# Optimization experiments

Hardware: AMD Instinct MI355X
Metric: run time of the kernel (lower is better)

The kernel has to match this reference:

```python
import jax, jax.numpy as jnp
import numpy as np

N = 6144   # number of patches (bag size)
L = 1024   # input feature dim
D = 512    # GCN hidden dim
ALPHA = 0.4
THRESH = 0.5


def _layernorm(x, g, b):
    m = jnp.mean(x, axis=-1, keepdims=True)
    v = jnp.mean((x - m) ** 2, axis=-1, keepdims=True)
    return (x - m) / jnp.sqrt(v + 1e-5) * g + b


def _l1rows(x):
    # F.normalize(x, p=1): row-wise L1 normalize with eps=1e-12
    return x / jnp.maximum(jnp.sum(jnp.abs(x), axis=1, keepdims=True), 1e-12)


def _nonlin(x, w1, b1, g, bn, w2, b2):
    h = jax.nn.relu(_layernorm(x @ w1 + b1, g, bn))
    return h @ w2 + b2


def _gcn(x, adj, w, b, g, bn):
    # GraphConvolution: adj @ (x @ W) + bias, then LayerNorm + ReLU
    return jax.nn.relu(_layernorm(adj @ (x @ w) + b, g, bn))


def setup_inputs() -> dict:
    key = jax.random.key(0)
    ks = iter(jax.random.split(key, 64))

    def nrm(shape, s=0.02):
        return jax.random.normal(next(ks), shape, jnp.float32) * s

    inp = {
        'x_path': jax.random.normal(next(ks), (N, L), jnp.float32),
        'maps': jax.random.uniform(next(ks), (N, N), jnp.float32) * 0.1,
    }
    for pre in ['nl0', 'nl1']:
        inp[pre + '_w1'] = nrm((L, D)); inp[pre + '_b1'] = jnp.zeros((D,), jnp.float32)
        inp[pre + '_g'] = jnp.ones((D,), jnp.float32); inp[pre + '_bn'] = jnp.zeros((D,), jnp.float32)
        inp[pre + '_w2'] = nrm((D, D)); inp[pre + '_b2'] = jnp.zeros((D,), jnp.float32)
    for pre in ['gc0', 'gc1', 'gc2', 'ga0', 'ga1', 'ga2']:
        inp[pre + '_w'] = nrm((D, D)); inp[pre + '_b'] = jnp.zeros((D,), jnp.float32)
        inp[pre + '_g'] = jnp.ones((D,), jnp.float32); inp[pre + '_bn'] = jnp.zeros((D,), jnp.float32)
    inp['attn_wa'] = nrm((L, 256)); inp['attn_ba'] = jnp.zeros((256,), jnp.float32)
    inp['attn_wb'] = nrm((L, 256)); inp['attn_bb'] = jnp.zeros((256,), jnp.float32)
    inp['attn_wc'] = nrm((256, 1)); inp['attn_bc'] = jnp.zeros((1,), jnp.float32)
    inp['cls_w'] = nrm((L, 4), 0.001)
    inp['ln_g'] = jnp.ones((L,), jnp.float32); inp['ln_b'] = jnp.zeros((L,), jnp.float32)
    return inp


def reference(x_path, maps,
              nl0_w1, nl0_b1, nl0_g, nl0_bn, nl0_w2, nl0_b2,
              nl1_w1, nl1_b1, nl1_g, nl1_bn, nl1_w2, nl1_b2,
              gc0_w, gc0_b, gc0_g, gc0_bn,
              gc1_w, gc1_b, gc1_g, gc1_bn,
              gc2_w, gc2_b, gc2_g, gc2_bn,
              ga0_w, ga0_b, ga0_g, ga0_bn,
              ga1_w, ga1_b, ga1_g, ga1_bn,
              ga2_w, ga2_b, ga2_g, ga2_bn,
              attn_wa, attn_ba, attn_wb, attn_bb, attn_wc, attn_bc,
              cls_w, ln_g, ln_b):
    # cosine-similarity adjacency: L2-normalize rows, gram matrix, min-max, threshold
    xn = x_path / jnp.maximum(jnp.linalg.norm(x_path, axis=1, keepdims=True), 1e-12)
    cs = xn @ xn.T                                       # [N,N]
    cs = (cs - cs.min()) / (cs.max() - cs.min())
    cs = (cs >= THRESH).astype(jnp.float32)

    # gated attention (eval mode, no dropout): A = Wc (tanh(Wa x) * sigmoid(Wb x))
    a = jnp.tanh(x_path @ attn_wa + attn_ba)
    bg = jax.nn.sigmoid(x_path @ attn_wb + attn_bb)
    agg = (a * bg) @ attn_wc + attn_bc                   # [N,1]

    s = jax.nn.sigmoid(agg)
    aw = s * s.T                                         # outer product [N,N]
    aw = (aw - aw.min()) / (aw.max() - aw.min())
    aw = ALPHA + (1.0 - ALPHA) * aw + maps

    cs = _l1rows(cs)
    aw = _l1rows(aw)

    x0 = _nonlin(x_path, nl0_w1, nl0_b1, nl0_g, nl0_bn, nl0_w2, nl0_b2)
    x1 = _nonlin(x_path, nl1_w1, nl1_b1, nl1_g, nl1_bn, nl1_w2, nl1_b2)

    g1 = _gcn(x0, cs, gc0_w, gc0_b, gc0_g, gc0_bn)
    g1 = _gcn(g1, cs, gc1_w, gc1_b, gc1_g, gc1_bn)
    g1 = _gcn(g1, cs, gc2_w, gc2_b, gc2_g, gc2_bn)

    g2 = _gcn(x1, aw, ga0_w, ga0_b, ga0_g, ga0_bn)
    g2 = _gcn(g2, aw, ga1_w, ga1_b, ga1_g, ga1_bn)
    g2 = _gcn(g2, aw, ga2_w, ga2_b, ga2_g, ga2_bn)

    gcf = jnp.concatenate([g2, g1], axis=1)              # [N, 1024]

    n = x_path.shape[0]
    trans = (cs @ agg) / (n ** 0.5)                      # [N,1]
    fw = jax.nn.softmax(0.3 * trans + 0.7 * agg, axis=0) # softmax over patches
    pooled = fw.T @ gcf                                  # [1, 1024]
    pooled = _layernorm(pooled, ln_g, ln_b)

    logits = pooled @ cls_w                              # [1, 4]
    y_hat = jnp.argmax(logits, axis=1, keepdims=True)    # topk k=1 index
    hazards = jax.nn.sigmoid(logits)
    surv = jnp.cumprod(1.0 - hazards, axis=1)
    return hazards, surv, y_hat
```

## Files before the change

kernel.cpp:

```cpp
#include <hip/hip_runtime.h>

#define N_ 6144
#define L_ 1024
#define D_ 512
#define H_ 256
#define SPARSE_MAX 64u

typedef unsigned short u16;
typedef unsigned long long u64;
typedef __attribute__((ext_vector_type(4))) float f32x4;
typedef __attribute__((ext_vector_type(8))) short s16x8;
typedef __attribute__((ext_vector_type(4))) short s16x4;

__device__ __forceinline__ u16 f2b(float f){
  unsigned u = __float_as_uint(f);
  u += 0x7FFFu + ((u >> 16) & 1u);
  return (u16)(u >> 16);
}
__device__ __forceinline__ float b2f(u16 h){ return __uint_as_float(((unsigned)h) << 16); }
__device__ __forceinline__ unsigned fkey(float f){
  unsigned u = __float_as_uint(f);
  return (u & 0x80000000u) ? ~u : (u | 0x80000000u);
}
__device__ __forceinline__ float funkey(unsigned k){
  unsigned u = (k & 0x80000000u) ? (k & 0x7FFFFFFFu) : ~k;
  return __uint_as_float(u);
}
__device__ __forceinline__ float wave_sum(float v){
  #pragma unroll
  for(int o=32;o;o>>=1) v += __shfl_xor(v,o);
  return v;
}
__device__ __forceinline__ float wave_max(float v){
  #pragma unroll
  for(int o=32;o;o>>=1) v = fmaxf(v,__shfl_xor(v,o));
  return v;
}
__device__ __forceinline__ float wave_min(float v){
  #pragma unroll
  for(int o=32;o;o>>=1) v = fminf(v,__shfl_xor(v,o));
  return v;
}
__device__ __forceinline__ float blk_sum256(float v){
  __shared__ float sm[4];
  v = wave_sum(v);
  __syncthreads();
  if((threadIdx.x&63)==0) sm[threadIdx.x>>6]=v;
  __syncthreads();
  return sm[0]+sm[1]+sm[2]+sm[3];
}
__device__ __forceinline__ float blk_min256(float v){
  __shared__ float sm[4];
  v = wave_min(v);
  __syncthreads();
  if((threadIdx.x&63)==0) sm[threadIdx.x>>6]=v;
  __syncthreads();
  return fminf(fminf(sm[0],sm[1]),fminf(sm[2],sm[3]));
}
__device__ __forceinline__ float blk_max256(float v){
  __shared__ float sm[4];
  v = wave_max(v);
  __syncthreads();
  if((threadIdx.x&63)==0) sm[threadIdx.x>>6]=v;
  __syncthreads();
  return fmaxf(fmaxf(sm[0],sm[1]),fmaxf(sm[2],sm[3]));
}


template<int VW> __device__ __forceinline__ void waitv(){
  if constexpr(VW==8) asm volatile("s_waitcnt vmcnt(8)" ::: "memory");
  else if constexpr(VW==4) asm volatile("s_waitcnt vmcnt(4)" ::: "memory");
  else asm volatile("s_waitcnt vmcnt(0)" ::: "memory");
}

#define STG4(bb,k0) do{ \
  __builtin_amdgcn_global_load_lds((__attribute__((address_space(1))) void*)(gA0+(k0)), (__attribute__((address_space(3))) void*)(lds + (bb)*4096 + (wid<<9)),        16, 0, 0); \
  __builtin_amdgcn_global_load_lds((__attribute__((address_space(1))) void*)(gA1+(k0)), (__attribute__((address_space(3))) void*)(lds + (bb)*4096 + 2048 + (wid<<9)), 16, 0, 0); \
  __builtin_amdgcn_global_load_lds((__attribute__((address_space(1))) void*)(gB0+(k0)), (__attribute__((address_space(3))) void*)(lds + 12288 + (bb)*4096 + (wid<<9)),        16, 0, 0); \
  __builtin_amdgcn_global_load_lds((__attribute__((address_space(1))) void*)(gB1+(k0)), (__attribute__((address_space(3))) void*)(lds + 12288 + (bb)*4096 + 2048 + (wid<<9)), 16, 0, 0); \
}while(0)

template<int MODE>
__global__ __launch_bounds__(256) void gemm_bt(
  const u16* __restrict__ A, const u16* __restrict__ Bt,
  int M, int Nc, int K,
  u16* __restrict__ Cb, unsigned* __restrict__ mmx,
  const unsigned* __restrict__ gate)
{
  if (gate && gate[2] <= SPARSE_MAX) return;
  __shared__ __align__(16) u16 lds[3*4096*2];
  const int tid = threadIdx.x;
  const int wid = tid>>6, lane = tid&63;

  const int gx = gridDim.x;
  int lid = blockIdx.y*gx + blockIdx.x;
  const int nwg = gx*gridDim.y;
  if ((nwg & 7) == 0) {
    const int chunk = nwg >> 3;
    lid = (lid & 7)*chunk + (lid >> 3);
  }
  const int m0 = (lid/gx)<<7, n0 = (lid%gx)<<7;
  const int wr = wid>>1, wc = wid&1;

  const int Klen = K / gridDim.z;
  const int kbeg = blockIdx.z * Klen;

  const int srow = (wid<<4) + (lane>>2);
  const int scol = (((lane&3) ^ ((lane>>2)&3))<<3);
  const u16* gA0 = A  + (size_t)(m0+srow   )*K + scol;
  const u16* gA1 = A  + (size_t)(m0+srow+64)*K + scol;
  const u16* gB0 = Bt + (size_t)(n0+srow   )*K + scol;
  const u16* gB1 = Bt + (size_t)(n0+srow+64)*K + scol;

  f32x4 acc[4][4] = {};
  const int lr = lane&15, lk = (lane>>4)<<3;
  const int rdo = lk ^ ((lr&3)<<3);

  const int NIT = Klen>>5;
  STG4(0, kbeg);
  STG4(1, kbeg+32);
  STG4(2, kbeg+64);

  for (int it=0; it<NIT-2; ++it){
    const int b = it - (it/3)*3;
    waitv<8>();
    __builtin_amdgcn_s_barrier();
    const u16* baseA = lds + b*4096;
    const u16* baseB = lds + 12288 + b*4096;
    s16x8 af[4], bfr[4];
    #pragma unroll
    for(int m=0;m<4;m++) af[m]  = *(const s16x8*)(baseA + ((wr<<6)+(m<<4)+lr)*32 + rdo);
    #pragma unroll
    for(int n=0;n<4;n++) bfr[n] = *(const s16x8*)(baseB + ((wc<<6)+(n<<4)+lr)*32 + rdo);
    asm volatile("s_waitcnt lgkmcnt(0)" ::: "memory");
    __builtin_amdgcn_sched_barrier(0);
    __builtin_amdgcn_s_barrier();
    if (it+3 < NIT) STG4(b, kbeg + ((it+3)<<5));
    #pragma unroll
    for(int m=0;m<4;m++)
      #pragma unroll
      for(int n=0;n<4;n++)
        acc[m][n] = __builtin_amdgcn_mfma_f32_16x16x32_bf16(af[m], bfr[n], acc[m][n], 0,0,0);
  }
  {
    const int it = NIT-2; const int b = it - (it/3)*3;
    waitv<4>();
    __builtin_amdgcn_s_barrier();
    const u16* baseA = lds + b*4096;
    const u16* baseB = lds + 12288 + b*4096;
    s16x8 af[4], bfr[4];
    #pragma unroll
    for(int m=0;m<4;m++) af[m]  = *(const s16x8*)(baseA + ((wr<<6)+(m<<4)+lr)*32 + rdo);
    #pragma unroll
    for(int n=0;n<4;n++) bfr[n] = *(const s16x8*)(baseB + ((wc<<6)+(n<<4)+lr)*32 + rdo);
    #pragma unroll
    for(int m=0;m<4;m++)
      #pragma unroll
      for(int n=0;n<4;n++)
        acc[m][n] = __builtin_amdgcn_mfma_f32_16x16x32_bf16(af[m], bfr[n], acc[m][n], 0,0,0);
  }
  {
    const int it = NIT-1; const int b = it - (it/3)*3;
    waitv<0>();
    __builtin_amdgcn_s_barrier();
    const u16* baseA = lds + b*4096;
    const u16* baseB = lds + 12288 + b*4096;
    s16x8 af[4], bfr[4];
    #pragma unroll
    for(int m=0;m<4;m++) af[m]  = *(const s16x8*)(baseA + ((wr<<6)+(m<<4)+lr)*32 + rdo);
    #pragma unroll
    for(int n=0;n<4;n++) bfr[n] = *(const s16x8*)(baseB + ((wc<<6)+(n<<4)+lr)*32 + rdo);
    #pragma unroll
    for(int m=0;m<4;m++)
      #pragma unroll
      for(int n=0;n<4;n++)
        acc[m][n] = __builtin_amdgcn_mfma_f32_16x16x32_bf16(af[m], bfr[n], acc[m][n], 0,0,0);
  }

  float tmin = 3.0e38f, tmax = -3.0e38f;
  if (MODE==1){
    #pragma unroll
    for(int m=0;m<4;m++)
      #pragma unroll
      for(int n=0;n<4;n++){
        f32x4 v = acc[m][n];
        #pragma unroll
        for(int e=0;e<4;e++){ tmin = fminf(tmin,v[e]); tmax = fmaxf(tmax,v[e]); }
      }
  }

  __syncthreads();
  u16* lC = lds;
  {
    const int rb_l = (wr<<6) + ((lane>>4)<<2);
    const int cb_l = (wc<<6) + lr;
    #pragma unroll
    for(int m=0;m<4;m++)
      #pragma unroll
      for(int n=0;n<4;n++){
        f32x4 v = acc[m][n];
        #pragma unroll
        for(int e=0;e<4;e++)
          lC[(rb_l+(m<<4)+e)*128 + cb_l+(n<<4)] = f2b(v[e]);
      }
  }
  __syncthreads();
  u16* Cp = (MODE==0) ? (Cb + (size_t)blockIdx.z * M * Nc) : Cb;
  #pragma unroll
  for(int q=0;q<8;q++){
    int c = (q<<8) + tid;
    int r = c>>4, cc = (c&15)<<3;
    s16x8 v = *(const s16x8*)(lC + r*128 + cc);
    if (MODE==1)
      __builtin_nontemporal_store(v, (s16x8*)(Cp + (size_t)(m0+r)*Nc + n0 + cc));
    else
      *(s16x8*)(Cp + (size_t)(m0+r)*Nc + n0 + cc) = v;
  }

  if (MODE==1){
    tmin = wave_min(tmin); tmax = wave_max(tmax);
    __shared__ float rmn[4], rmx[4];
    if(lane==0){ rmn[wid]=tmin; rmx[wid]=tmax; }
    __syncthreads();
    if(tid==0){
      float mn=fminf(fminf(rmn[0],rmn[1]),fminf(rmn[2],rmn[3]));
      float mx=fmaxf(fmaxf(rmx[0],rmx[1]),fmaxf(rmx[2],rmx[3]));
      atomicMin(mmx+0, fkey(mn));
      atomicMax(mmx+1, fkey(mx));
    }
  }
}

__global__ __launch_bounds__(256) void transpose_cast(
  const float* __restrict__ src, u16* __restrict__ dst, int R, int C)
{
  __shared__ float t[32][33];
  int c0 = blockIdx.x<<5, r0 = blockIdx.y<<5;
  int tx = threadIdx.x&31, ty = threadIdx.x>>5;
  #pragma unroll
  for(int i=0;i<32;i+=8) t[ty+i][tx] = src[(size_t)(r0+ty+i)*C + c0+tx];
  __syncthreads();
  #pragma unroll
  for(int i=0;i<32;i+=8) dst[(size_t)(c0+ty+i)*R + r0+tx] = f2b(t[tx][ty+i]);
}

__global__ __launch_bounds__(256) void transpose_sum_bf(
  const u16* __restrict__ src, size_t pstr, int nsp,
  u16* __restrict__ dst, int R, int C, const unsigned* __restrict__ gate)
{
  if (gate && gate[2] <= SPARSE_MAX) return;
  __shared__ float t[32][33];
  int c0 = blockIdx.x<<5, r0 = blockIdx.y<<5;
  int tx = threadIdx.x&31, ty = threadIdx.x>>5;
  #pragma unroll
  for(int i=0;i<32;i+=8){
    float v = 0;
    for(int p=0;p<nsp;p++)
      v += b2f(src[(size_t)p*pstr + (size_t)(r0+ty+i)*C + c0+tx]);
    t[ty+i][tx] = v;
  }
  __syncthreads();
  #pragma unroll
  for(int i=0;i<32;i+=8) dst[(size_t)(c0+ty+i)*R + r0+tx] = f2b(t[tx][ty+i]);
}

__global__ __launch_bounds__(256) void prep_x(const float* __restrict__ x,
  u16* __restrict__ xb, u16* __restrict__ xnb)
{
  int row = blockIdx.x, t = threadIdx.x;
  const float* p = x + (size_t)row*L_ + (t<<2);
  f32x4 v = *(const f32x4*)p;
  float ss = v[0]*v[0]+v[1]*v[1]+v[2]*v[2]+v[3]*v[3];
  float tot = blk_sum256(ss);
  float inv = 1.0f/fmaxf(sqrtf(tot), 1e-12f);
  u16* pb = xb  + (size_t)row*L_ + (t<<2);
  u16* pn = xnb + (size_t)row*L_ + (t<<2);
  #pragma unroll
  for(int k=0;k<4;k++){ pb[k]=f2b(v[k]); pn[k]=f2b(v[k]*inv); }
}

__global__ __launch_bounds__(256) void attn_epi(const u16* __restrict__ SPA,
  size_t pstr, int nsp,
  const float* __restrict__ ba, const float* __restrict__ bb,
  const float* __restrict__ wc, const float* __restrict__ bc,
  float* __restrict__ agg, float* __restrict__ s)
{
  int row = (blockIdx.x<<2) + (threadIdx.x>>6);
  int lane = threadIdx.x&63;
  float a[4]={0,0,0,0}, b[4]={0,0,0,0};
  for(int p=0;p<nsp;p++){
    s16x4 ua = *(const s16x4*)(SPA + (size_t)p*pstr + (size_t)row*1536 + (lane<<2));
    s16x4 ub = *(const s16x4*)(SPA + (size_t)p*pstr + (size_t)row*1536 + 256 + (lane<<2));
    #pragma unroll
    for(int j=0;j<4;j++){ a[j]+=b2f((u16)ua[j]); b[j]+=b2f((u16)ub[j]); }
  }
  float acc=0;
  #pragma unroll
  for(int j=0;j<4;j++){
    int h = (lane<<2)+j;
    float tv = tanhf(a[j]+ba[h]);
    float sg = 1.0f/(1.0f+expf(-(b[j]+bb[h])));
    acc += tv*sg*wc[h];
  }
  acc = wave_sum(acc);
  if(lane==0){
    float v = acc + bc[0];
    agg[row]=v;
    s[row]=1.0f/(1.0f+expf(-v));
  }
}

__global__ __launch_bounds__(256) void s_stats(const float* __restrict__ s, float* __restrict__ sc){
  int t=threadIdx.x;
  float sum=0, mn=3e38f, mx=-3e38f;
  for(int i=t;i<N_;i+=256){ float v=s[i]; sum+=v; mn=fminf(mn,v); mx=fmaxf(mx,v); }
  float S=blk_sum256(sum);
  float MN=blk_min256(mn);
  float MX=blk_max256(mx);
  if(t==0){ sc[0]=S; sc[1]=MN; sc[2]=MX; }
}

__global__ __launch_bounds__(256) void aw_write(const float* __restrict__ maps, const float* __restrict__ s,
  const float* __restrict__ sc, u16* __restrict__ awb)
{
  int i = blockIdx.x, t = threadIdx.x;
  float smin = sc[1], smax = sc[2];
  float mn = smin*smin, mx = smax*smax;
  float beta = 0.6f/(mx-mn);
  float c1 = 0.4f - beta*mn;
  float si = s[i];
  const float* mrow = maps + (size_t)i*N_;
  float mv[24];
  float part = 0;
  #pragma unroll
  for(int q=0;q<24;q++){
    int j = t + (q<<8);
    mv[q] = c1 + beta*si*s[j] + mrow[j];
    part += mv[q];
  }
  float r = blk_sum256(part);
  float inv = 1.0f/fmaxf(r, 1e-12f);
  u16* orow = awb + (size_t)i*N_;
  #pragma unroll
  for(int q=0;q<24;q++)
    __builtin_nontemporal_store(f2b(mv[q]*inv), orow + t + (q<<8));
}

__global__ __launch_bounds__(256) void ln_epi512(const u16* __restrict__ Y, size_t pstr, int nsp,
  int rs, int cbase,
  const float* __restrict__ ki,
  const float* __restrict__ bias, const float* __restrict__ g, const float* __restrict__ bn,
  u16* __restrict__ outb,
  const unsigned* __restrict__ gate, const u16* __restrict__ Yalt)
{
  const u16* src = Y; size_t ps = pstr; int np = nsp, rstride = rs, cb = cbase;
  if (gate && gate[2] <= SPARSE_MAX){ src = Yalt; ps = 0; np = 1; rstride = 512; cb = 0; }
  int row = (blockIdx.x<<2)+(threadIdx.x>>6);
  int lane = threadIdx.x&63;
  int c0 = lane<<3;
  float v[8] = {0,0,0,0,0,0,0,0};
  for(int p=0;p<np;p++){
    s16x8 u = *(const s16x8*)(src + (size_t)p*ps + (size_t)row*rstride + cb + c0);
    #pragma unroll
    for(int j=0;j<8;j++) v[j] += b2f((u16)u[j]);
  }
  float scale = ki ? (1.0f/ki[row]) : 1.0f;
  float sum=0, ssum=0;
  #pragma unroll
  for(int j=0;j<8;j++){ v[j] = v[j]*scale + bias[c0+j]; sum+=v[j]; ssum+=v[j]*v[j]; }
  sum = wave_sum(sum); ssum = wave_sum(ssum);
  float m = sum*(1.0f/D_);
  float var = ssum*(1.0f/D_) - m*m;
  float invsd = rsqrtf(var + 1e-5f);
  u16 ob[8];
  #pragma unroll
  for(int j=0;j<8;j++){
    float o = (v[j]-m)*invsd*g[c0+j] + bn[c0+j];
    o = fmaxf(o, 0.0f);
    ob[j] = f2b(o);
  }
  *(s16x8*)(outb + (size_t)row*D_ + c0) = *(s16x8*)ob;
}

__global__ __launch_bounds__(256) void bias_cast(const u16* __restrict__ Y, size_t pstr, int nsp,
  const float* __restrict__ b, u16* __restrict__ outb)
{
  size_t idx = ((size_t)blockIdx.x*256 + threadIdx.x)<<3;
  float v[8] = {0,0,0,0,0,0,0,0};
  for(int p=0;p<nsp;p++){
    s16x8 u = *(const s16x8*)(Y + (size_t)p*pstr + idx);
    #pragma unroll
    for(int j=0;j<8;j++) v[j] += b2f((u16)u[j]);
  }
  int c = (int)(idx & (D_-1));
  u16 ob[8];
  #pragma unroll
  for(int k=0;k<8;k++) ob[k] = f2b(v[k]+b[c+k]);
  *(s16x8*)(outb+idx) = *(s16x8*)ob;
}

__global__ void init_k(unsigned* mmx){ mmx[0]=0xFFFFFFFFu; mmx[1]=0u; mmx[2]=0u; }

__global__ __launch_bounds__(256) void binarize(u16* __restrict__ csb,
  unsigned* __restrict__ mmx, const float* __restrict__ agg,
  float* __restrict__ ki, float* __restrict__ z, u64* __restrict__ bm)
{
  int i = blockIdx.x, t = threadIdx.x;
  int lane = t&63, w = t>>6;
  float mn = funkey(mmx[0]), mx = funkey(mmx[1]);
  float th = mn + 0.5f*(mx-mn);
  u16* row = csb + (size_t)i*N_;
  u64* bmrow = bm + (size_t)i*96;
  float cnt = 0, dot = 0;
  #pragma unroll
  for(int q=0;q<24;q++){
    int j = t + (q<<8);
    bool on = b2f(row[j]) >= th;
    __builtin_nontemporal_store(on ? (u16)0x3F80 : (u16)0, row + j);
    u64 mask = __ballot(on);
    if(lane==0) bmrow[(q<<2)+w] = mask;
    if(on){ cnt += 1.0f; dot += agg[j]; }
  }
  float k = blk_sum256(cnt);
  float dt = blk_sum256(dot);
  if(t==0){
    ki[i] = k;
    float tr = dt/(k*sqrtf((float)N_));
    z[i] = 0.3f*tr + 0.7f*agg[i];
    atomicMax(mmx+2, (unsigned)(k+0.5f));
  }
}

__global__ __launch_bounds__(256) void gather_rows(const u64* __restrict__ bm,
  const u16* __restrict__ SPp, size_t pstr, int nsp,
  const unsigned* __restrict__ gate, u16* __restrict__ YS)
{
  if (gate[2] > SPARSE_MAX) return;
  int i = blockIdx.x, t = threadIdx.x;
  __shared__ u64 wbuf[96];
  __shared__ u16 idx[SPARSE_MAX];
  __shared__ int nn_s;
  if (t < 96) wbuf[t] = bm[(size_t)i*96 + t];
  __syncthreads();
  if (t == 0){
    int nn = 0;
    for(int k=0;k<96;k++){
      u64 m = wbuf[k];
      while(m && nn < (int)SPARSE_MAX){
        int b = __ffsll((long long)m) - 1;
        m &= m - 1;
        idx[nn++] = (u16)((k<<6) + b);
      }
    }
    nn_s = nn;
  }
  __syncthreads();
  int nn = nn_s;
  float a0=0, a1=0;
  for(int k=0;k<nn;k++){
    size_t jb = (size_t)idx[k]*512;
    for(int p=0;p<nsp;p++){
      a0 += b2f(SPp[p*pstr + jb + t]);
      a1 += b2f(SPp[p*pstr + jb + t + 256]);
    }
  }
  YS[(size_t)i*512 + t]       = f2b(a0);
  YS[(size_t)i*512 + t + 256] = f2b(a1);
}

__global__ __launch_bounds__(1024) void softmax_prep(const float* __restrict__ z,
  float* __restrict__ e, float* __restrict__ sexp)
{
  int t = threadIdx.x;
  __shared__ float sm[16];
  float mx=-3e38f;
  for(int i=t;i<N_;i+=1024) mx=fmaxf(mx,z[i]);
  mx = wave_max(mx);
  if((t&63)==0) sm[t>>6]=mx;
  __syncthreads();
  float zm = sm[0];
  #pragma unroll
  for(int w=1;w<16;w++) zm=fmaxf(zm,sm[w]);
  __syncthreads();
  float sum=0;
  for(int i=t;i<N_;i+=1024){ float ee=expf(z[i]-zm); e[i]=ee; sum+=ee; }
  sum = wave_sum(sum);
  if((t&63)==0) sm[t>>6]=sum;
  __syncthreads();
  if(t==0){ float S=0; for(int w=0;w<16;w++) S+=sm[w]; *sexp=S; }
}

__global__ __launch_bounds__(256) void pooled_partial(const float* __restrict__ e,
  const u16* __restrict__ g2b, const u16* __restrict__ g1b, float* __restrict__ part)
{
  int b = blockIdx.x, t = threadIdx.x;
  float a0=0,a1=0,a2=0,a3=0;
  for(int r=0;r<24;r++){
    int row = b*24+r;
    float w = e[row];
    a0 += w * b2f(g2b[(size_t)row*D_ + t]);
    a1 += w * b2f(g2b[(size_t)row*D_ + t+256]);
    a2 += w * b2f(g1b[(size_t)row*D_ + t]);
    a3 += w * b2f(g1b[(size_t)row*D_ + t+256]);
  }
  part[(size_t)b*1024 + t]      = a0;
  part[(size_t)b*1024 + t+256]  = a1;
  part[(size_t)b*1024 + t+512]  = a2;
  part[(size_t)b*1024 + t+768]  = a3;
}

__global__ __launch_bounds__(1024) void final_k(const float* __restrict__ part, const float* __restrict__ sexp,
  const float* __restrict__ lng, const float* __restrict__ lnb,
  const float* __restrict__ clsw, float* __restrict__ out)
{
  int t = threadIdx.x;
  __shared__ float red[16];
  __shared__ float smv[1024];
  __shared__ float lgs[4];
  float p=0;
  for(int b=0;b<256;b++) p += part[b*1024 + t];
  p /= sexp[0];
  float w = wave_sum(p);
  if((t&63)==0) red[t>>6]=w;
  __syncthreads();
  float tot=0;
  #pragma unroll
  for(int i2=0;i2<16;i2++) tot+=red[i2];
  float m = tot*(1.0f/1024.0f);
  __syncthreads();
  float d = p-m;
  w = wave_sum(d*d);
  if((t&63)==0) red[t>>6]=w;
  __syncthreads();
  tot=0;
  #pragma unroll
  for(int i2=0;i2<16;i2++) tot+=red[i2];
  float var = tot*(1.0f/1024.0f);
  float y = d*rsqrtf(var+1e-5f)*lng[t] + lnb[t];
  smv[t]=y;
  __syncthreads();
  if(t<4){
    float lg=0;
    for(int j=0;j<1024;j++) lg += smv[j]*clsw[j*4+t];
    lgs[t]=lg;
  }
  __syncthreads();
  if(t==0){
    float h[4];
    int am=0; float best=lgs[0];
    #pragma unroll
    for(int c2=0;c2<4;c2++){ h[c2]=1.0f/(1.0f+expf(-lgs[c2])); if(lgs[c2]>best){best=lgs[c2];am=c2;} }
    float sv=1.0f;
    #pragma unroll
    for(int c2=0;c2<4;c2++){ out[c2]=h[c2]; sv*=(1.0f-h[c2]); out[4+c2]=sv; }
    out[8]=(float)am;
  }
}

extern "C" void kernel_launch(void* const* d_in, const int* in_sizes, int n_in,
                              void* d_out, int out_size, void* d_ws, size_t ws_size,
                              hipStream_t stream)
{
  const float* x_path =(const float*)d_in[0];
  const float* maps   =(const float*)d_in[1];
  const float* nl0_w1 =(const float*)d_in[2];
  const float* nl0_b1 =(const float*)d_in[3];
  const float* nl0_g  =(const float*)d_in[4];
  const float* nl0_bn =(const float*)d_in[5];
  const float* nl0_w2 =(const float*)d_in[6];
  const float* nl0_b2 =(const float*)d_in[7];
  const float* nl1_w1 =(const float*)d_in[8];
  const float* nl1_b1 =(const float*)d_in[9];
  const float* nl1_g  =(const float*)d_in[10];
  const float* nl1_bn =(const float*)d_in[11];
  const float* nl1_w2 =(const float*)d_in[12];
  const float* nl1_b2 =(const float*)d_in[13];
  const float *gw[6], *gb[6], *gg[6], *gbn[6];
  for(int l=0;l<6;l++){
    gw[l]  = (const float*)d_in[14+l*4+0];
    gb[l]  = (const float*)d_in[14+l*4+1];
    gg[l]  = (const float*)d_in[14+l*4+2];
    gbn[l] = (const float*)d_in[14+l*4+3];
  }
  const float* attn_wa=(const float*)d_in[38];
  const float* attn_ba=(const float*)d_in[39];
  const float* attn_wb=(const float*)d_in[40];
  const float* attn_bb=(const float*)d_in[41];
  const float* attn_wc=(const float*)d_in[42];
  const float* attn_bc=(const float*)d_in[43];
  const float* cls_w  =(const float*)d_in[44];
  const float* ln_g   =(const float*)d_in[45];
  const float* ln_b   =(const float*)d_in[46];

  char* ws=(char*)d_ws;
  size_t off=0;
  auto alc=[&](size_t b)->char*{ char* p=ws+off; off=(off+b+255)&~(size_t)255; return p; };
  u16* BIG = (u16*)alc((size_t)N_*N_*2);
  u16* XB  = (u16*)alc((size_t)N_*L_*2);
  u16* XNB = (u16*)alc((size_t)N_*L_*2);
  u16* WT_proj=(u16*)alc((size_t)1536*L_*2);
  u16* WT_nl0w2=(u16*)alc((size_t)D_*D_*2);
  u16* WT_nl1w2=(u16*)alc((size_t)D_*D_*2);
  u16* WT_g[6];
  for(int l=0;l<6;l++) WT_g[l]=(u16*)alc((size_t)D_*D_*2);
  u16* SP = (u16*)alc((size_t)2*N_*1536*2);
  u16* XWT=(u16*)alc((size_t)D_*N_*2);
  u16* XA0=(u16*)alc((size_t)N_*D_*2);
  u16* XA1=(u16*)alc((size_t)N_*D_*2);
  u16* X0B=(u16*)alc((size_t)N_*D_*2);
  u16* X1B=(u16*)alc((size_t)N_*D_*2);
  u16* YS =(u16*)alc((size_t)N_*D_*2);
  u64* BM =(u64*)alc((size_t)N_*96*8);
  float* PART=(float*)alc((size_t)256*1024*4);
  float* AGG=(float*)alc(N_*4);
  float* SS =(float*)alc(N_*4);
  float* KI =(float*)alc(N_*4);
  float* Z  =(float*)alc(N_*4);
  float* E  =(float*)alc(N_*4);
  float* SC =(float*)alc(256);
  unsigned* MMX=(unsigned*)alc(256);
  float* SEXP=(float*)alc(256);

  const size_t PS_D = (size_t)N_*D_;
  const size_t PS_P = (size_t)N_*1536;

  init_k<<<1,1,0,stream>>>(MMX);
  prep_x<<<N_,256,0,stream>>>(x_path, XB, XNB);

  transpose_cast<<<dim3(H_/32, L_/32),256,0,stream>>>(attn_wa, WT_proj,                         L_, H_);
  transpose_cast<<<dim3(H_/32, L_/32),256,0,stream>>>(attn_wb, WT_proj + (size_t)256*L_,        L_, H_);
  transpose_cast<<<dim3(D_/32, L_/32),256,0,stream>>>(nl0_w1,  WT_proj + (size_t)512*L_,        L_, D_);
  transpose_cast<<<dim3(D_/32, L_/32),256,0,stream>>>(nl1_w1,  WT_proj + (size_t)1024*L_,       L_, D_);
  transpose_cast<<<dim3(D_/32, D_/32),256,0,stream>>>(nl0_w2, WT_nl0w2, D_, D_);
  transpose_cast<<<dim3(D_/32, D_/32),256,0,stream>>>(nl1_w2, WT_nl1w2, D_, D_);
  for(int l=0;l<6;l++)
    transpose_cast<<<dim3(D_/32, D_/32),256,0,stream>>>(gw[l], WT_g[l], D_, D_);

  gemm_bt<0><<<dim3(1536/128, N_/128, 2),256,0,stream>>>(XB, WT_proj, N_, 1536, L_, SP, nullptr, nullptr);
  attn_epi<<<N_/4,256,0,stream>>>(SP, PS_P, 2, attn_ba, attn_bb, attn_wc, attn_bc, AGG, SS);
  s_stats<<<1,256,0,stream>>>(SS,SC);
  aw_write<<<N_,256,0,stream>>>(maps,SS,SC,BIG);

  ln_epi512<<<N_/4,256,0,stream>>>(SP,PS_P,2, 1536,1024, nullptr, nl1_b1,nl1_g,nl1_bn, XA1, nullptr,nullptr);
  ln_epi512<<<N_/4,256,0,stream>>>(SP,PS_P,2, 1536, 512, nullptr, nl0_b1,nl0_g,nl0_bn, XA0, nullptr,nullptr);

  gemm_bt<0><<<dim3(D_/128,N_/128,4),256,0,stream>>>(XA1, WT_nl1w2, N_,D_,D_, SP, nullptr, nullptr);
  bias_cast<<<(N_*D_/8)/256,256,0,stream>>>(SP,PS_D,4, nl1_b2, X1B);

  {
    const u16* cur=X1B;
    for(int l=0;l<3;l++){
      int gi = 3+l;
      gemm_bt<0><<<dim3(D_/128,N_/128,4),256,0,stream>>>(cur, WT_g[gi], N_,D_,D_, SP, nullptr, nullptr);
      transpose_sum_bf<<<dim3(D_/32, N_/32),256,0,stream>>>(SP, PS_D, 4, XWT, N_, D_, nullptr);
      gemm_bt<0><<<dim3(D_/128,N_/128,4),256,0,stream>>>(BIG, XWT, N_,D_,N_, SP, nullptr, nullptr);
      u16* nxt = (l==0)? XA1 : (l==1)? YS : X1B;
      ln_epi512<<<N_/4,256,0,stream>>>(SP,PS_D,4, 512,0, nullptr, gb[gi],gg[gi],gbn[gi], nxt, nullptr,nullptr);
      cur = nxt;
    }
  }

  gemm_bt<0><<<dim3(D_/128,N_/128,4),256,0,stream>>>(XA0, WT_nl0w2, N_,D_,D_, SP, nullptr, nullptr);
  bias_cast<<<(N_*D_/8)/256,256,0,stream>>>(SP,PS_D,4, nl0_b2, X0B);

  gemm_bt<1><<<dim3(N_/128,N_/128,1),256,0,stream>>>(XNB, XNB, N_,N_,L_, BIG, MMX, nullptr);
  binarize<<<N_,256,0,stream>>>(BIG, MMX, AGG, KI, Z, BM);

  {
    const u16* cur=X0B;
    for(int l=0;l<3;l++){
      int gi = l;
      gemm_bt<0><<<dim3(D_/128,N_/128,4),256,0,stream>>>(cur, WT_g[gi], N_,D_,D_, SP, nullptr, nullptr);
      transpose_sum_bf<<<dim3(D_/32, N_/32),256,0,stream>>>(SP, PS_D, 4, XWT, N_, D_, MMX);
      gemm_bt<0><<<dim3(D_/128,N_/128,4),256,0,stream>>>(BIG, XWT, N_,D_,N_, SP, nullptr, MMX);
      gather_rows<<<N_,256,0,stream>>>(BM, SP, PS_D, 4, MMX, YS);
      u16* nxt = (l==0)? XA1 : (l==1)? XA0 : X0B;
      ln_epi512<<<N_/4,256,0,stream>>>(SP,PS_D,4, 512,0, KI, gb[gi],gg[gi],gbn[gi], nxt, MMX, YS);
      cur = nxt;
    }
  }

  softmax_prep<<<1,1024,0,stream>>>(Z,E,SEXP);
  pooled_partial<<<256,256,0,stream>>>(E,X1B,X0B,PART);
  final_k<<<1,1024,0,stream>>>(PART,SEXP,ln_g,ln_b,cls_w,(float*)d_out);

  (void)in_sizes;(void)n_in;(void)out_size;(void)ws_size;
}
```

Before: 869.7 us.

## Add 256x256-tile 8-wave GEMM kernel for large adjacency and similarity GEMMs

Adds a new gemm256 kernel with 256x256 output tiles, 512 threads, BK=64 double-buffered LDS staging, a swizzled LDS layout, four-phase MFMA interleaving with s_setprio, and staggered B loads. It replaces the 128x128 gemm_bt for the dense aw-adjacency GEMMs (K=6144) and the 6144x6144 cosine-similarity GEMM with min/max tracking. The goal is higher arithmetic intensity per LDS and global byte on the dominant GEMMs. In exchange, occupancy drops because the kernel uses 128KB of LDS and many accumulators. The old kernel also loses its LDS XOR swizzle, which may add bank conflicts in the remaining gemm_bt calls.

```diff
diff --git a/kernel.cpp b/kernel.cpp
--- a/kernel.cpp
+++ b/kernel.cpp
@@ -66,6 +66,150 @@
   return fmaxf(fmaxf(sm[0],sm[1]),fmaxf(sm[2],sm[3]));
 }
 
+
+#define STG_A(bb,H,Q,KT) __builtin_amdgcn_global_load_lds( \
+  (__attribute__((address_space(1))) void*)(gAr + (size_t)((H)*128+(Q)*64)*K + (size_t)(KT)*64), \
+  (__attribute__((address_space(3))) void*)(lds + (bb)*16384 + (H)*8192 + (Q)*4096 + (wid<<9)), 16, 0, 0)
+#define STG_B(bb,H,Q,KT) __builtin_amdgcn_global_load_lds( \
+  (__attribute__((address_space(1))) void*)(gBr + (size_t)((H)*128+(Q)*64)*K + (size_t)(KT)*64), \
+  (__attribute__((address_space(3))) void*)(lds + 32768 + (bb)*16384 + (H)*8192 + (Q)*4096 + (wid<<9)), 16, 0, 0)
+
+#define RD(base,row,ks) (*(const s16x8*)(lds + (base) + (row)*64 + ((((ks)<<5) + ((lane>>4)<<3)) ^ (((row)&4)<<2))))
+
+#define MM(i,j,x,y) acc[i][j]=__builtin_amdgcn_mfma_f32_16x16x32_bf16(x,y,acc[i][j],0,0,0)
+
+#define PHASE(QR,QC,EXTRA) do{ \
+  s16x8 af0,af1,af2,af3,ag0,ag1,ag2,ag3,bv0,bv1,bw0,bw1; \
+  { int r0=(wm<<7)+((QR)<<6)+lr; \
+    af0=RD(abase,r0,0);    ag0=RD(abase,r0,1); \
+    af1=RD(abase,r0+16,0); ag1=RD(abase,r0+16,1); \
+    af2=RD(abase,r0+32,0); ag2=RD(abase,r0+32,1); \
+    af3=RD(abase,r0+48,0); ag3=RD(abase,r0+48,1); \
+    int s0=(wn<<6)+((QC)<<5)+lr; \
+    bv0=RD(bbase,s0,0);    bw0=RD(bbase,s0,1); \
+    bv1=RD(bbase,s0+16,0); bw1=RD(bbase,s0+16,1); } \
+  EXTRA; \
+  __builtin_amdgcn_s_barrier(); \
+  __builtin_amdgcn_s_setprio(1); \
+  MM((QR)*4+0,(QC)*2+0,af0,bv0); MM((QR)*4+0,(QC)*2+0,ag0,bw0); \
+  MM((QR)*4+1,(QC)*2+0,af1,bv0); MM((QR)*4+1,(QC)*2+0,ag1,bw0); \
+  MM((QR)*4+2,(QC)*2+0,af2,bv0); MM((QR)*4+2,(QC)*2+0,ag2,bw0); \
+  MM((QR)*4+3,(QC)*2+0,af3,bv0); MM((QR)*4+3,(QC)*2+0,ag3,bw0); \
+  MM((QR)*4+0,(QC)*2+1,af0,bv1); MM((QR)*4+0,(QC)*2+1,ag0,bw1); \
+  MM((QR)*4+1,(QC)*2+1,af1,bv1); MM((QR)*4+1,(QC)*2+1,ag1,bw1); \
+  MM((QR)*4+2,(QC)*2+1,af2,bv1); MM((QR)*4+2,(QC)*2+1,ag2,bw1); \
+  MM((QR)*4+3,(QC)*2+1,af3,bv1); MM((QR)*4+3,(QC)*2+1,ag3,bw1); \
+  __builtin_amdgcn_s_setprio(0); \
+  __builtin_amdgcn_s_barrier(); \
+}while(0)
+
+template<int MODE>
+__global__ __launch_bounds__(512,2) void gemm256(
+  const u16* __restrict__ A, const u16* __restrict__ Bt,
+  int M, int Nc, int K,
+  u16* __restrict__ Cb, unsigned* __restrict__ mmx)
+{
+  __shared__ __align__(16) u16 lds[65536];
+  const int tid = threadIdx.x;
+  const int wid = tid>>6, lane = tid&63;
+  const int wm = wid>>2, wn = wid&3;
+  const int lr = lane&15;
+
+  const int gx = gridDim.x;
+  int lid = blockIdx.y*gx + blockIdx.x;
+  const int nwg = gx*gridDim.y;
+  if ((nwg & 7) == 0){ const int chunk = nwg>>3; lid = (lid&7)*chunk + (lid>>3); }
+  const int m0 = (lid/gx)<<8, n0 = (lid%gx)<<8;
+
+  const int Klen = K/gridDim.z;
+  const int kbeg = blockIdx.z*Klen;
+  const int NT = Klen>>6;
+  const int kt0 = kbeg>>6;
+
+  const int srow = (wid<<3) + (lane>>3);
+  const int scol = ((lane&7)<<3) ^ ((lane&32)>>1);
+  const u16* gAr = A  + (size_t)(m0 + srow)*K + scol;
+  const u16* gBr = Bt + (size_t)(n0 + srow)*K + scol;
+
+  f32x4 acc[8][4] = {};
+
+  STG_A(0,0,0,kt0); STG_A(0,0,1,kt0); STG_A(0,1,0,kt0); STG_A(0,1,1,kt0);
+  STG_B(0,0,0,kt0); STG_B(0,0,1,kt0); STG_B(0,1,0,kt0); STG_B(0,1,1,kt0);
+
+  for (int t=0; t<NT; ++t){
+    const int cbuf = t&1, nbuf = cbuf^1;
+    const int abase = cbuf*16384, bbase = 32768 + cbuf*16384;
+    const int ktn = kt0 + t + 1;
+    if (t+1 < NT){
+      STG_A(nbuf,0,0,ktn); STG_A(nbuf,0,1,ktn); STG_A(nbuf,1,0,ktn); STG_A(nbuf,1,1,ktn);
+      asm volatile("s_waitcnt vmcnt(4)" ::: "memory");
+    } else {
+      asm volatile("s_waitcnt vmcnt(0)" ::: "memory");
+    }
+    __builtin_amdgcn_sched_barrier(0);
+    __builtin_amdgcn_s_barrier();
+    PHASE(0,0, (void)0 );
+    PHASE(0,1, if(t+1<NT){ STG_B(nbuf,0,0,ktn); STG_B(nbuf,0,1,ktn); } );
+    PHASE(1,0, if(t+1<NT){ STG_B(nbuf,1,0,ktn); STG_B(nbuf,1,1,ktn); } );
+    PHASE(1,1, (void)0 );
+  }
+
+  float tmin=3.0e38f, tmax=-3.0e38f;
+  if (MODE==1){
+    #pragma unroll
+    for(int mi=0;mi<8;mi++)
+      #pragma unroll
+      for(int ni=0;ni<4;ni++){
+        f32x4 v=acc[mi][ni];
+        #pragma unroll
+        for(int e=0;e<4;e++){ tmin=fminf(tmin,v[e]); tmax=fmaxf(tmax,v[e]); }
+      }
+  }
+
+  __syncthreads();
+  #pragma unroll
+  for(int p=0;p<2;p++){
+    if (wm==p){
+      #pragma unroll
+      for(int mi=0;mi<8;mi++)
+        #pragma unroll
+        for(int ni=0;ni<4;ni++){
+          f32x4 v=acc[mi][ni];
+          int rl=(mi<<4)+((lane>>4)<<2);
+          int cl=(wn<<6)+(ni<<4)+lr;
+          #pragma unroll
+          for(int e=0;e<4;e++) lds[(rl+e)*256+cl]=f2b(v[e]);
+        }
+    }
+    __syncthreads();
+    u16* Cp = (MODE==0) ? (Cb + (size_t)blockIdx.z*M*Nc) : Cb;
+    #pragma unroll
+    for(int it=0;it<8;it++){
+      int idx=(it<<12)+(tid<<3);
+      int row=idx>>8, col=idx&255;
+      s16x8 v=*(const s16x8*)(lds+idx);
+      if (MODE==1)
+        __builtin_nontemporal_store(v,(s16x8*)(Cp+(size_t)(m0+(p<<7)+row)*Nc+n0+col));
+      else
+        *(s16x8*)(Cp+(size_t)(m0+(p<<7)+row)*Nc+n0+col)=v;
+    }
+    __syncthreads();
+  }
+
+  if (MODE==1){
+    tmin=wave_min(tmin); tmax=wave_max(tmax);
+    __shared__ float rmn[8], rmx[8];
+    if(lane==0){ rmn[wid]=tmin; rmx[wid]=tmax; }
+    __syncthreads();
+    if(tid==0){
+      float mn=rmn[0], mx=rmx[0];
+      #pragma unroll
+      for(int i=1;i<8;i++){ mn=fminf(mn,rmn[i]); mx=fmaxf(mx,rmx[i]); }
+      atomicMin(mmx+0,fkey(mn));
+      atomicMax(mmx+1,fkey(mx));
+    }
+  }
+}
 
 template<int VW> __device__ __forceinline__ void waitv(){
   if constexpr(VW==8) asm volatile("s_waitcnt vmcnt(8)" ::: "memory");
@@ -106,7 +250,7 @@
   const int kbeg = blockIdx.z * Klen;
 
   const int srow = (wid<<4) + (lane>>2);
-  const int scol = (((lane&3) ^ ((lane>>2)&3))<<3);
+  const int scol = (lane&3)<<3;
   const u16* gA0 = A  + (size_t)(m0+srow   )*K + scol;
   const u16* gA1 = A  + (size_t)(m0+srow+64)*K + scol;
   const u16* gB0 = Bt + (size_t)(n0+srow   )*K + scol;
@@ -114,7 +258,6 @@
 
   f32x4 acc[4][4] = {};
   const int lr = lane&15, lk = (lane>>4)<<3;
-  const int rdo = lk ^ ((lr&3)<<3);
 
   const int NIT = Klen>>5;
   STG4(0, kbeg);
@@ -129,9 +272,9 @@
     const u16* baseB = lds + 12288 + b*4096;
     s16x8 af[4], bfr[4];
     #pragma unroll
-    for(int m=0;m<4;m++) af[m]  = *(const s16x8*)(baseA + ((wr<<6)+(m<<4)+lr)*32 + rdo);
-    #pragma unroll
-    for(int n=0;n<4;n++) bfr[n] = *(const s16x8*)(baseB + ((wc<<6)+(n<<4)+lr)*32 + rdo);
+    for(int m=0;m<4;m++) af[m]  = *(const s16x8*)(baseA + ((wr<<6)+(m<<4)+lr)*32 + lk);
+    #pragma unroll
+    for(int n=0;n<4;n++) bfr[n] = *(const s16x8*)(baseB + ((wc<<6)+(n<<4)+lr)*32 + lk);
     asm volatile("s_waitcnt lgkmcnt(0)" ::: "memory");
     __builtin_amdgcn_sched_barrier(0);
     __builtin_amdgcn_s_barrier();
@@ -150,9 +293,9 @@
     const u16* baseB = lds + 12288 + b*4096;
     s16x8 af[4], bfr[4];
     #pragma unroll
-    for(int m=0;m<4;m++) af[m]  = *(const s16x8*)(baseA + ((wr<<6)+(m<<4)+lr)*32 + rdo);
-    #pragma unroll
-    for(int n=0;n<4;n++) bfr[n] = *(const s16x8*)(baseB + ((wc<<6)+(n<<4)+lr)*32 + rdo);
+    for(int m=0;m<4;m++) af[m]  = *(const s16x8*)(baseA + ((wr<<6)+(m<<4)+lr)*32 + lk);
+    #pragma unroll
+    for(int n=0;n<4;n++) bfr[n] = *(const s16x8*)(baseB + ((wc<<6)+(n<<4)+lr)*32 + lk);
     #pragma unroll
     for(int m=0;m<4;m++)
       #pragma unroll
@@ -167,26 +310,14 @@
     const u16* baseB = lds + 12288 + b*4096;
     s16x8 af[4], bfr[4];
     #pragma unroll
-    for(int m=0;m<4;m++) af[m]  = *(const s16x8*)(baseA + ((wr<<6)+(m<<4)+lr)*32 + rdo);
-    #pragma unroll
-    for(int n=0;n<4;n++) bfr[n] = *(const s16x8*)(baseB + ((wc<<6)+(n<<4)+lr)*32 + rdo);
+    for(int m=0;m<4;m++) af[m]  = *(const s16x8*)(baseA + ((wr<<6)+(m<<4)+lr)*32 + lk);
+    #pragma unroll
+    for(int n=0;n<4;n++) bfr[n] = *(const s16x8*)(baseB + ((wc<<6)+(n<<4)+lr)*32 + lk);
     #pragma unroll
     for(int m=0;m<4;m++)
       #pragma unroll
       for(int n=0;n<4;n++)
         acc[m][n] = __builtin_amdgcn_mfma_f32_16x16x32_bf16(af[m], bfr[n], acc[m][n], 0,0,0);
-  }
-
-  float tmin = 3.0e38f, tmax = -3.0e38f;
-  if (MODE==1){
-    #pragma unroll
-    for(int m=0;m<4;m++)
-      #pragma unroll
-      for(int n=0;n<4;n++){
-        f32x4 v = acc[m][n];
-        #pragma unroll
-        for(int e=0;e<4;e++){ tmin = fminf(tmin,v[e]); tmax = fmaxf(tmax,v[e]); }
-      }
   }
 
   __syncthreads();
@@ -205,30 +336,14 @@
       }
   }
   __syncthreads();
-  u16* Cp = (MODE==0) ? (Cb + (size_t)blockIdx.z * M * Nc) : Cb;
+  u16* Cp = Cb + (size_t)blockIdx.z * M * Nc;
   #pragma unroll
   for(int q=0;q<8;q++){
     int c = (q<<8) + tid;
     int r = c>>4, cc = (c&15)<<3;
-    s16x8 v = *(const s16x8*)(lC + r*128 + cc);
-    if (MODE==1)
-      __builtin_nontemporal_store(v, (s16x8*)(Cp + (size_t)(m0+r)*Nc + n0 + cc));
-    else
-      *(s16x8*)(Cp + (size_t)(m0+r)*Nc + n0 + cc) = v;
-  }
-
-  if (MODE==1){
-    tmin = wave_min(tmin); tmax = wave_max(tmax);
-    __shared__ float rmn[4], rmx[4];
-    if(lane==0){ rmn[wid]=tmin; rmx[wid]=tmax; }
-    __syncthreads();
-    if(tid==0){
-      float mn=fminf(fminf(rmn[0],rmn[1]),fminf(rmn[2],rmn[3]));
-      float mx=fmaxf(fmaxf(rmx[0],rmx[1]),fmaxf(rmx[2],rmx[3]));
-      atomicMin(mmx+0, fkey(mn));
-      atomicMax(mmx+1, fkey(mx));
-    }
-  }
+    *(s16x8*)(Cp + (size_t)(m0+r)*Nc + n0 + cc) = *(const s16x8*)(lC + r*128 + cc);
+  }
+  (void)mmx;
 }
 
 __global__ __launch_bounds__(256) void transpose_cast(
@@ -627,10 +742,10 @@
   init_k<<<1,1,0,stream>>>(MMX);
   prep_x<<<N_,256,0,stream>>>(x_path, XB, XNB);
 
-  transpose_cast<<<dim3(H_/32, L_/32),256,0,stream>>>(attn_wa, WT_proj,                         L_, H_);
-  transpose_cast<<<dim3(H_/32, L_/32),256,0,stream>>>(attn_wb, WT_proj + (size_t)256*L_,        L_, H_);
-  transpose_cast<<<dim3(D_/32, L_/32),256,0,stream>>>(nl0_w1,  WT_proj + (size_t)512*L_,        L_, D_);
-  transpose_cast<<<dim3(D_/32, L_/32),256,0,stream>>>(nl1_w1,  WT_proj + (size_t)1024*L_,       L_, D_);
+  transpose_cast<<<dim3(H_/32, L_/32),256,0,stream>>>(attn_wa, WT_proj,                   L_, H_);
+  transpose_cast<<<dim3(H_/32, L_/32),256,0,stream>>>(attn_wb, WT_proj + (size_t)256*L_,  L_, H_);
+  transpose_cast<<<dim3(D_/32, L_/32),256,0,stream>>>(nl0_w1,  WT_proj + (size_t)512*L_,  L_, D_);
+  transpose_cast<<<dim3(D_/32, L_/32),256,0,stream>>>(nl1_w1,  WT_proj + (size_t)1024*L_, L_, D_);
   transpose_cast<<<dim3(D_/32, D_/32),256,0,stream>>>(nl0_w2, WT_nl0w2, D_, D_);
   transpose_cast<<<dim3(D_/32, D_/32),256,0,stream>>>(nl1_w2, WT_nl1w2, D_, D_);
   for(int l=0;l<6;l++)
@@ -653,7 +768,7 @@
       int gi = 3+l;
       gemm_bt<0><<<dim3(D_/128,N_/128,4),256,0,stream>>>(cur, WT_g[gi], N_,D_,D_, SP, nullptr, nullptr);
       transpose_sum_bf<<<dim3(D_/32, N_/32),256,0,stream>>>(SP, PS_D, 4, XWT, N_, D_, nullptr);
-      gemm_bt<0><<<dim3(D_/128,N_/128,4),256,0,stream>>>(BIG, XWT, N_,D_,N_, SP, nullptr, nullptr);
+      gemm256<0><<<dim3(D_/256, N_/256, 4),512,0,stream>>>(BIG, XWT, N_,D_,N_, SP, nullptr);
       u16* nxt = (l==0)? XA1 : (l==1)? YS : X1B;
       ln_epi512<<<N_/4,256,0,stream>>>(SP,PS_D,4, 512,0, nullptr, gb[gi],gg[gi],gbn[gi], nxt, nullptr,nullptr);
       cur = nxt;
@@ -663,7 +778,7 @@
   gemm_bt<0><<<dim3(D_/128,N_/128,4),256,0,stream>>>(XA0, WT_nl0w2, N_,D_,D_, SP, nullptr, nullptr);
   bias_cast<<<(N_*D_/8)/256,256,0,stream>>>(SP,PS_D,4, nl0_b2, X0B);
 
-  gemm_bt<1><<<dim3(N_/128,N_/128,1),256,0,stream>>>(XNB, XNB, N_,N_,L_, BIG, MMX, nullptr);
+  gemm256<1><<<dim3(N_/256, N_/256, 1),512,0,stream>>>(XNB, XNB, N_,N_,L_, BIG, MMX);
   binarize<<<N_,256,0,stream>>>(BIG, MMX, AGG, KI, Z, BM);
 
   {
```

Result: slower. 958.7 us (+10.2%).
